# Kernel optimization log

Hardware: AMD Instinct MI355X
Metric: run time of the kernel (lower is better)

## Reference

```python
import jax, jax.numpy as jnp
import numpy as np

N = 1000000
E = 16000000


def gcn_conv(x, W, b, src, dst, dinv_sqrt):
    # x: [N, Cin]; W: [Cin, Cout]; src/dst: [E'] (self-loops included)
    xw = x @ W                                   # [N, Cout]
    norm = dinv_sqrt[src] * dinv_sqrt[dst]       # [E']
    msg = xw[src] * norm[:, None]                # [E', Cout]
    out = jax.ops.segment_sum(msg, dst, num_segments=x.shape[0])
    return out + b


def setup_inputs() -> dict:
    key = jax.random.key(0)
    ks = jax.random.split(key, 8)
    x = jax.random.normal(ks[0], (N, 1), dtype=jnp.float32)
    edge_index = jax.random.randint(ks[1], (2, E), 0, N, dtype=jnp.int64)
    W1 = jax.random.normal(ks[2], (1, 3), dtype=jnp.float32)
    b1 = jax.random.normal(ks[3], (3,), dtype=jnp.float32) * 0.1
    W2 = jax.random.normal(ks[4], (3, 3), dtype=jnp.float32) * 0.5
    b2 = jax.random.normal(ks[5], (3,), dtype=jnp.float32) * 0.1
    W3 = jax.random.normal(ks[6], (3, 3), dtype=jnp.float32) * 0.5
    b3 = jax.random.normal(ks[7], (3,), dtype=jnp.float32) * 0.1
    return {"x": x, "edge_index": edge_index, "W1": W1, "b1": b1,
            "W2": W2, "b2": b2, "W3": W3, "b3": b3}


def reference(x, edge_index, W1, b1, W2, b2, W3, b3):
    n = x.shape[0]
    # add self-loops (PyG GCNConv default)
    loop = jnp.arange(n, dtype=edge_index.dtype)
    src = jnp.concatenate([edge_index[0], loop])
    dst = jnp.concatenate([edge_index[1], loop])
    # symmetric normalization: deg over targets of A + I
    deg = jax.ops.segment_sum(jnp.ones_like(dst, dtype=x.dtype), dst, num_segments=n)
    dinv_sqrt = jnp.where(deg > 0, jax.lax.rsqrt(deg), 0.0)
    h = jax.nn.relu(gcn_conv(x, W1, b1, src, dst, dinv_sqrt))
    h = jax.nn.relu(gcn_conv(h, W2, b2, src, dst, dinv_sqrt))
    h = jax.nn.relu(gcn_conv(h, W3, b3, src, dst, dinv_sqrt))
    return h
```

## Files before the change

### kernel.cpp

```cpp
#include <hip/hip_runtime.h>

#define THREADS 256
#define TILE 8192
#define TPB_S 512
#define EPT 16
#define BUCKET_BITS 10
#define BUCKET_SIZE 1024
#define NT_MAX 2048
#define STAGE_CAP 17152

__device__ __forceinline__ long long llmin(long long a, long long b) { return a < b ? a : b; }


__global__ void detect_i64_kernel(const int* __restrict__ e, int* __restrict__ flag) {
    if (blockIdx.x == 0 && threadIdx.x == 0) {
        bool all_odd_zero = true, any_even = false;
#pragma unroll
        for (int k = 0; k < 16; ++k) {
            if (e[2 * k + 1] != 0) all_odd_zero = false;
            if (e[2 * k] != 0) any_even = true;
        }
        *flag = (all_odd_zero && any_even) ? 1 : 0;
    }
}


__global__ __launch_bounds__(TPB_S) void binsort_kernel(
        const int* __restrict__ e, long long E, const int* __restrict__ flag,
        int nbuck, int* __restrict__ packed, int* __restrict__ ofs) {
    __shared__ int hist[1024];
    __shared__ int sarr[TPB_S];
    __shared__ int srec[TILE];
    const int tid = threadIdx.x;
    hist[tid] = 0;
    hist[tid + TPB_S] = 0;
    __syncthreads();

    const bool i64 = (*flag != 0);
    const long long beg = (long long)blockIdx.x * TILE;
    const int tile_len = (int)llmin((long long)TILE, E - beg);

    int rec[EPT];
    int bkt[EPT];
#pragma unroll
    for (int k = 0; k < EPT; ++k) {
        int j = tid + k * TPB_S;
        bkt[k] = -1;
        if (j < tile_len) {
            long long idx = beg + j;
            int s, d;
            if (i64) { s = ((const int2*)e)[idx].x; d = ((const int2*)e)[E + idx].x; }
            else     { s = e[idx];                  d = e[E + idx]; }
            bkt[k] = d >> BUCKET_BITS;
            rec[k] = ((d & (BUCKET_SIZE - 1)) << 20) | s;
            atomicAdd(&hist[bkt[k]], 1);
        }
    }
    __syncthreads();

    int v0 = hist[2 * tid], v1 = hist[2 * tid + 1];
    sarr[tid] = v0 + v1;
    __syncthreads();
    for (int off = 1; off < TPB_S; off <<= 1) {
        int t = (tid >= off) ? sarr[tid - off] : 0;
        __syncthreads();
        sarr[tid] += t;
        __syncthreads();
    }
    int excl = (tid == 0) ? 0 : sarr[tid - 1];
    hist[2 * tid] = excl;
    hist[2 * tid + 1] = excl + v0;
    __syncthreads();

    int* orow = ofs + (size_t)blockIdx.x * nbuck;
    if (tid < nbuck) orow[tid] = hist[tid];
    if (tid + TPB_S < nbuck) orow[tid + TPB_S] = hist[tid + TPB_S];
    __syncthreads();

#pragma unroll
    for (int k = 0; k < EPT; ++k) {
        if (bkt[k] >= 0) {
            int pos = atomicAdd(&hist[bkt[k]], 1);
            srec[pos] = rec[k];
        }
    }
    __syncthreads();

    int* prow = packed + (size_t)blockIdx.x * TILE;
    for (int j = tid; j < tile_len; j += TPB_S) prow[j] = srec[j];
}

#define TRT 32
__global__ void transpose_kernel(const int* __restrict__ in, int rows, int cols,
                                 int* __restrict__ outT) {
    __shared__ int tb[TRT][TRT + 1];
    int c0 = blockIdx.x * TRT, r0 = blockIdx.y * TRT;
    int lx = threadIdx.x, ly = threadIdx.y;
    for (int dy = ly; dy < TRT; dy += 8) {
        int r = r0 + dy, c = c0 + lx;
        if (r < rows && c < cols) tb[dy][lx] = in[(size_t)r * cols + c];
    }
    __syncthreads();
    for (int dy = ly; dy < TRT; dy += 8) {
        int r = c0 + dy, c = r0 + lx;
        if (r < cols && c < rows) outT[(size_t)r * rows + c] = tb[lx][dy];
    }
}


__global__ __launch_bounds__(THREADS) void bcnt_kernel(
        const int* __restrict__ ofsT, long long E, int ntiles, int nbuck,
        int* __restrict__ bcnt) {
    __shared__ int sh[THREADS];
    const int b = blockIdx.x, tid = threadIdx.x;
    const int* row0 = ofsT + (size_t)b * ntiles;
    const int* row1 = row0 + ntiles;
    const bool last_b = (b == nbuck - 1);
    int s = 0;
    for (int t = tid; t < ntiles; t += THREADS) {
        int o = row0[t];
        int tl = (t == ntiles - 1) ? (int)(E - (long long)t * TILE) : TILE;
        int o2 = last_b ? tl : row1[t];
        s += o2 - o;
    }
    sh[tid] = s;
    __syncthreads();
    for (int off = THREADS >> 1; off > 0; off >>= 1) {
        if (tid < off) sh[tid] += sh[tid + off];
        __syncthreads();
    }
    if (tid == 0) bcnt[b] = sh[0];
}

__global__ __launch_bounds__(1024) void bscan_kernel(
        const int* __restrict__ bcnt, int nbuck, int* __restrict__ bs) {
    __shared__ int sh[1024];
    int tid = threadIdx.x;
    int v = (tid < nbuck) ? bcnt[tid] : 0;
    sh[tid] = v;
    __syncthreads();
    for (int off = 1; off < 1024; off <<= 1) {
        int t = (tid >= off) ? sh[tid - off] : 0;
        __syncthreads();
        sh[tid] += t;
        __syncthreads();
    }
    if (tid < nbuck) bs[tid] = sh[tid] - v;
    if (tid == nbuck - 1) bs[nbuck] = sh[tid];
}


__global__ __launch_bounds__(TPB_S) void merge_kernel(
        const int* __restrict__ ofsT, const int* __restrict__ packed,
        const int* __restrict__ bs, long long E, int ntiles, int nbuck,
        int* __restrict__ merged) {
    __shared__ int lofs[NT_MAX];
    __shared__ int tsum[TPB_S];
    __shared__ int stage[STAGE_CAP];
    const int tid = threadIdx.x, b = blockIdx.x;
    const int* row0 = ofsT + (size_t)b * ntiles;
    const int* row1 = row0 + ntiles;
    const bool last_b = (b == nbuck - 1);
    const int per = (ntiles + TPB_S - 1) / TPB_S;
    const int t0 = tid * per;

    int s = 0;
    for (int k = 0; k < per; ++k) {
        int t = t0 + k;
        if (t < ntiles) {
            int o = row0[t];
            int tl = (t == ntiles - 1) ? (int)(E - (long long)t * TILE) : TILE;
            int o2 = last_b ? tl : row1[t];
            lofs[t] = s;
            s += o2 - o;
        }
    }
    tsum[tid] = s;
    __syncthreads();
    for (int off = 1; off < TPB_S; off <<= 1) {
        int t = (tid >= off) ? tsum[tid - off] : 0;
        __syncthreads();
        tsum[tid] += t;
        __syncthreads();
    }
    const int excl = tsum[tid] - s;
    const int total = tsum[TPB_S - 1];
    for (int k = 0; k < per; ++k) {
        int t = t0 + k;
        if (t < ntiles) lofs[t] += excl;
    }
    __syncthreads();

    const int bsb = bs[b];
    for (int k = 0; k < per; ++k) {
        int t = t0 + k;
        if (t >= ntiles) break;
        int o = row0[t];
        int tl = (t == ntiles - 1) ? (int)(E - (long long)t * TILE) : TILE;
        int o2 = last_b ? tl : row1[t];
        const int* pr = packed + (size_t)t * TILE;
        int q = lofs[t];
        int j = o;
        for (; j + 4 <= o2; j += 4, q += 4) {
            int a0 = pr[j], a1 = pr[j + 1], a2 = pr[j + 2], a3 = pr[j + 3];
            if (q + 3 < STAGE_CAP) {
                stage[q] = a0; stage[q + 1] = a1; stage[q + 2] = a2; stage[q + 3] = a3;
            } else {
                if (q < STAGE_CAP) stage[q] = a0; else merged[bsb + q] = a0;
                if (q + 1 < STAGE_CAP) stage[q + 1] = a1; else merged[bsb + q + 1] = a1;
                if (q + 2 < STAGE_CAP) stage[q + 2] = a2; else merged[bsb + q + 2] = a2;
                merged[bsb + q + 3] = a3;
            }
        }
        for (; j < o2; ++j, ++q) {
            int a0 = pr[j];
            if (q < STAGE_CAP) stage[q] = a0; else merged[bsb + q] = a0;
        }
    }
    __syncthreads();

    const int wlen = total < STAGE_CAP ? total : STAGE_CAP;
    for (int j = tid; j < wlen; j += TPB_S) merged[bsb + j] = stage[j];
}


__global__ void deg_init_kernel(const int* __restrict__ bs, const int* __restrict__ packed,
                                const float* __restrict__ x,
                                float* __restrict__ dinv, float* __restrict__ p, int N) {
    __shared__ int cnt[BUCKET_SIZE];
    for (int k = threadIdx.x; k < BUCKET_SIZE; k += blockDim.x) cnt[k] = 0;
    __syncthreads();
    int beg = bs[blockIdx.x], end = bs[blockIdx.x + 1];
    int stride = blockDim.x;
    int k = beg + threadIdx.x;
    for (; k + 3 * stride < end; k += 4 * stride) {
        unsigned r0 = packed[k], r1 = packed[k + stride];
        unsigned r2 = packed[k + 2 * stride], r3 = packed[k + 3 * stride];
        atomicAdd(&cnt[r0 >> 20], 1);
        atomicAdd(&cnt[r1 >> 20], 1);
        atomicAdd(&cnt[r2 >> 20], 1);
        atomicAdd(&cnt[r3 >> 20], 1);
    }
    for (; k < end; k += stride) atomicAdd(&cnt[((unsigned)packed[k]) >> 20], 1);
    __syncthreads();
    int base = blockIdx.x << BUCKET_BITS;
    for (int j = threadIdx.x; j < BUCKET_SIZE; j += blockDim.x) {
        int i = base + j;
        if (i < N) {
            float di = rsqrtf((float)cnt[j] + 1.0f);
            dinv[i] = di;
            p[i] = x[i] * di;
        }
    }
}

__global__ void layer1_bucket_kernel(const int* __restrict__ bs, const int* __restrict__ packed,
                                     const float* __restrict__ p, const float* __restrict__ dinv,
                                     const float* __restrict__ W1, const float* __restrict__ b1,
                                     const float* __restrict__ W2,
                                     float4* __restrict__ y2, int N) {
    __shared__ float acc[BUCKET_SIZE];
    for (int k = threadIdx.x; k < BUCKET_SIZE; k += blockDim.x) acc[k] = 0.0f;
    __syncthreads();
    int beg = bs[blockIdx.x], end = bs[blockIdx.x + 1];
    int stride = blockDim.x;
    int k = beg + threadIdx.x;
    for (; k + 3 * stride < end; k += 4 * stride) {
        unsigned r0 = packed[k], r1 = packed[k + stride];
        unsigned r2 = packed[k + 2 * stride], r3 = packed[k + 3 * stride];
        float v0 = p[r0 & 0xFFFFFu], v1 = p[r1 & 0xFFFFFu];
        float v2 = p[r2 & 0xFFFFFu], v3 = p[r3 & 0xFFFFFu];
        atomicAdd(&acc[r0 >> 20], v0);
        atomicAdd(&acc[r1 >> 20], v1);
        atomicAdd(&acc[r2 >> 20], v2);
        atomicAdd(&acc[r3 >> 20], v3);
    }
    for (; k < end; k += stride) {
        unsigned rec = (unsigned)packed[k];
        atomicAdd(&acc[rec >> 20], p[rec & 0xFFFFFu]);
    }
    __syncthreads();
    int base = blockIdx.x << BUCKET_BITS;
    for (int j = threadIdx.x; j < BUCKET_SIZE; j += blockDim.x) {
        int i = base + j;
        if (i >= N) continue;
        float di = dinv[i];
        float t = di * (acc[j] + p[i]);
        float h0 = fmaxf(t * W1[0] + b1[0], 0.0f);
        float h1 = fmaxf(t * W1[1] + b1[1], 0.0f);
        float h2 = fmaxf(t * W1[2] + b1[2], 0.0f);
        float4 o;
        o.x = di * (h0 * W2[0] + h1 * W2[3] + h2 * W2[6]);
        o.y = di * (h0 * W2[1] + h1 * W2[4] + h2 * W2[7]);
        o.z = di * (h0 * W2[2] + h1 * W2[5] + h2 * W2[8]);
        o.w = 0.0f;
        y2[i] = o;
    }
}

__global__ void layer_mid_bucket_kernel(const int* __restrict__ bs, const int* __restrict__ packed,
                                        const float4* __restrict__ y, const float* __restrict__ dinv,
                                        const float* __restrict__ b, const float* __restrict__ Wn,
                                        float4* __restrict__ ynext, int N) {
    __shared__ float acc[BUCKET_SIZE * 3];
    for (int k = threadIdx.x; k < BUCKET_SIZE * 3; k += blockDim.x) acc[k] = 0.0f;
    __syncthreads();
    int beg = bs[blockIdx.x], end = bs[blockIdx.x + 1];
    int stride = blockDim.x;
    int k = beg + threadIdx.x;
    for (; k + 3 * stride < end; k += 4 * stride) {
        unsigned r0 = packed[k], r1 = packed[k + stride];
        unsigned r2 = packed[k + 2 * stride], r3 = packed[k + 3 * stride];
        float4 v0 = y[r0 & 0xFFFFFu], v1 = y[r1 & 0xFFFFFu];
        float4 v2 = y[r2 & 0xFFFFFu], v3 = y[r3 & 0xFFFFFu];
        int d0 = (r0 >> 20) * 3, d1 = (r1 >> 20) * 3, d2 = (r2 >> 20) * 3, d3 = (r3 >> 20) * 3;
        atomicAdd(&acc[d0 + 0], v0.x); atomicAdd(&acc[d0 + 1], v0.y); atomicAdd(&acc[d0 + 2], v0.z);
        atomicAdd(&acc[d1 + 0], v1.x); atomicAdd(&acc[d1 + 1], v1.y); atomicAdd(&acc[d1 + 2], v1.z);
        atomicAdd(&acc[d2 + 0], v2.x); atomicAdd(&acc[d2 + 1], v2.y); atomicAdd(&acc[d2 + 2], v2.z);
        atomicAdd(&acc[d3 + 0], v3.x); atomicAdd(&acc[d3 + 1], v3.y); atomicAdd(&acc[d3 + 2], v3.z);
    }
    for (; k < end; k += stride) {
        unsigned rec = (unsigned)packed[k];
        float4 v = y[rec & 0xFFFFFu];
        int dl = (rec >> 20) * 3;
        atomicAdd(&acc[dl + 0], v.x);
        atomicAdd(&acc[dl + 1], v.y);
        atomicAdd(&acc[dl + 2], v.z);
    }
    __syncthreads();
    int base = blockIdx.x << BUCKET_BITS;
    for (int j = threadIdx.x; j < BUCKET_SIZE; j += blockDim.x) {
        int i = base + j;
        if (i >= N) continue;
        float di = dinv[i];
        float4 yi = y[i];
        float h0 = fmaxf(di * (acc[j * 3 + 0] + yi.x) + b[0], 0.0f);
        float h1 = fmaxf(di * (acc[j * 3 + 1] + yi.y) + b[1], 0.0f);
        float h2 = fmaxf(di * (acc[j * 3 + 2] + yi.z) + b[2], 0.0f);
        float4 o;
        o.x = di * (h0 * Wn[0] + h1 * Wn[3] + h2 * Wn[6]);
        o.y = di * (h0 * Wn[1] + h1 * Wn[4] + h2 * Wn[7]);
        o.z = di * (h0 * Wn[2] + h1 * Wn[5] + h2 * Wn[8]);
        o.w = 0.0f;
        ynext[i] = o;
    }
}

__global__ void layer_last_bucket_kernel(const int* __restrict__ bs, const int* __restrict__ packed,
                                         const float4* __restrict__ y, const float* __restrict__ dinv,
                                         const float* __restrict__ b,
                                         float* __restrict__ out, int N) {
    __shared__ float acc[BUCKET_SIZE * 3];
    for (int k = threadIdx.x; k < BUCKET_SIZE * 3; k += blockDim.x) acc[k] = 0.0f;
    __syncthreads();
    int beg = bs[blockIdx.x], end = bs[blockIdx.x + 1];
    int stride = blockDim.x;
    int k = beg + threadIdx.x;
    for (; k + 3 * stride < end; k += 4 * stride) {
        unsigned r0 = packed[k], r1 = packed[k + stride];
        unsigned r2 = packed[k + 2 * stride], r3 = packed[k + 3 * stride];
        float4 v0 = y[r0 & 0xFFFFFu], v1 = y[r1 & 0xFFFFFu];
        float4 v2 = y[r2 & 0xFFFFFu], v3 = y[r3 & 0xFFFFFu];
        int d0 = (r0 >> 20) * 3, d1 = (r1 >> 20) * 3, d2 = (r2 >> 20) * 3, d3 = (r3 >> 20) * 3;
        atomicAdd(&acc[d0 + 0], v0.x); atomicAdd(&acc[d0 + 1], v0.y); atomicAdd(&acc[d0 + 2], v0.z);
        atomicAdd(&acc[d1 + 0], v1.x); atomicAdd(&acc[d1 + 1], v1.y); atomicAdd(&acc[d1 + 2], v1.z);
        atomicAdd(&acc[d2 + 0], v2.x); atomicAdd(&acc[d2 + 1], v2.y); atomicAdd(&acc[d2 + 2], v2.z);
        atomicAdd(&acc[d3 + 0], v3.x); atomicAdd(&acc[d3 + 1], v3.y); atomicAdd(&acc[d3 + 2], v3.z);
    }
    for (; k < end; k += stride) {
        unsigned rec = (unsigned)packed[k];
        float4 v = y[rec & 0xFFFFFu];
        int dl = (rec >> 20) * 3;
        atomicAdd(&acc[dl + 0], v.x);
        atomicAdd(&acc[dl + 1], v.y);
        atomicAdd(&acc[dl + 2], v.z);
    }
    __syncthreads();
    int base = blockIdx.x << BUCKET_BITS;
    for (int j = threadIdx.x; j < BUCKET_SIZE; j += blockDim.x) {
        int i = base + j;
        if (i >= N) continue;
        float di = dinv[i];
        float4 yi = y[i];
        out[i * 3 + 0] = fmaxf(di * (acc[j * 3 + 0] + yi.x) + b[0], 0.0f);
        out[i * 3 + 1] = fmaxf(di * (acc[j * 3 + 1] + yi.y) + b[1], 0.0f);
        out[i * 3 + 2] = fmaxf(di * (acc[j * 3 + 2] + yi.z) + b[2], 0.0f);
    }
}


__global__ void deg_kernel(const int* __restrict__ e, long long E,
                           const int* __restrict__ flag, float* __restrict__ deg) {
    const bool i64 = (*flag != 0);
    long long i = (long long)blockIdx.x * blockDim.x + threadIdx.x;
    const long long stride = (long long)gridDim.x * blockDim.x;
    for (; i < E; i += stride) {
        long long t = i64 ? (long long)e[2 * E + 2 * i] : (long long)e[E + i];
        atomicAdd(deg + t, 1.0f);
    }
}

__global__ void node_init_kernel(const float* __restrict__ x, const float* __restrict__ W1,
                                 float* __restrict__ deg_dinv, float* __restrict__ A, int N) {
    int i = blockIdx.x * blockDim.x + threadIdx.x;
    if (i >= N) return;
    float di = rsqrtf(deg_dinv[i] + 1.0f);
    deg_dinv[i] = di;
    float v = x[i] * di;
    A[i * 3 + 0] = v * W1[0];
    A[i * 3 + 1] = v * W1[1];
    A[i * 3 + 2] = v * W1[2];
}

__global__ void scatter_kernel(const int* __restrict__ e, long long E,
                               const int* __restrict__ flag,
                               const float* __restrict__ y, float* __restrict__ acc) {
    const bool i64 = (*flag != 0);
    long long i = (long long)blockIdx.x * blockDim.x + threadIdx.x;
    const long long stride = (long long)gridDim.x * blockDim.x;
    for (; i < E; i += stride) {
        int s, t;
        if (i64) { s = e[2 * i]; t = e[2 * E + 2 * i]; }
        else     { s = e[i];     t = e[E + i]; }
        atomicAdd(acc + (long long)t * 3 + 0, y[(long long)s * 3 + 0]);
        atomicAdd(acc + (long long)t * 3 + 1, y[(long long)s * 3 + 1]);
        atomicAdd(acc + (long long)t * 3 + 2, y[(long long)s * 3 + 2]);
    }
}

__global__ void finalize_mid_kernel(const float* __restrict__ dinv, const float* __restrict__ y,
                                    float* __restrict__ acc, const float* __restrict__ b,
                                    const float* __restrict__ Wn, int N) {
    int i = blockIdx.x * blockDim.x + threadIdx.x;
    if (i >= N) return;
    float di = dinv[i];
    float h0 = fmaxf(di * (acc[i * 3 + 0] + y[i * 3 + 0]) + b[0], 0.0f);
    float h1 = fmaxf(di * (acc[i * 3 + 1] + y[i * 3 + 1]) + b[1], 0.0f);
    float h2 = fmaxf(di * (acc[i * 3 + 2] + y[i * 3 + 2]) + b[2], 0.0f);
    float z0 = di * (h0 * Wn[0] + h1 * Wn[3] + h2 * Wn[6]);
    float z1 = di * (h0 * Wn[1] + h1 * Wn[4] + h2 * Wn[7]);
    float z2 = di * (h0 * Wn[2] + h1 * Wn[5] + h2 * Wn[8]);
    acc[i * 3 + 0] = z0;
    acc[i * 3 + 1] = z1;
    acc[i * 3 + 2] = z2;
}

__global__ void finalize_last_kernel(const float* __restrict__ dinv, const float* __restrict__ y,
                                     const float* __restrict__ acc, const float* __restrict__ b,
                                     float* __restrict__ out, int N) {
    int i = blockIdx.x * blockDim.x + threadIdx.x;
    if (i >= N) return;
    float di = dinv[i];
    out[i * 3 + 0] = fmaxf(di * (acc[i * 3 + 0] + y[i * 3 + 0]) + b[0], 0.0f);
    out[i * 3 + 1] = fmaxf(di * (acc[i * 3 + 1] + y[i * 3 + 1]) + b[1], 0.0f);
    out[i * 3 + 2] = fmaxf(di * (acc[i * 3 + 2] + y[i * 3 + 2]) + b[2], 0.0f);
}


extern "C" void kernel_launch(void* const* d_in, const int* in_sizes, int n_in,
                              void* d_out, int out_size, void* d_ws, size_t ws_size,
                              hipStream_t stream) {
    const float* x  = (const float*)d_in[0];
    const int*   ei = (const int*)d_in[1];
    const float* W1 = (const float*)d_in[2];
    const float* b1 = (const float*)d_in[3];
    const float* W2 = (const float*)d_in[4];
    const float* b2 = (const float*)d_in[5];
    const float* W3 = (const float*)d_in[6];
    const float* b3 = (const float*)d_in[7];
    float* out = (float*)d_out;

    const long long N = in_sizes[0];
    const long long E = (long long)in_sizes[1] / 2;

    const int nbuck  = (int)((N + BUCKET_SIZE - 1) >> BUCKET_BITS);
    const int ntiles = (int)((E + TILE - 1) / TILE);

    char* w = (char*)d_ws;
    size_t off = 0;
    auto alloc = [&](size_t bytes) -> char* {
        char* pp = w + off;
        off = (off + bytes + 255) & ~(size_t)255;
        return pp;
    };

    int*    flag   = (int*)alloc(4);
    int*    ofs    = (int*)alloc((size_t)ntiles * nbuck * 4);
    int*    ofsT   = (int*)alloc((size_t)nbuck * ntiles * 4);
    int*    bcnt   = (int*)alloc((size_t)nbuck * 4);
    int*    bs     = (int*)alloc(((size_t)nbuck + 1) * 4);
    int*    packed = (int*)alloc((size_t)ntiles * TILE * 4);
    int*    merged = (int*)alloc((size_t)E * 4);
    float*  dinv   = (float*)alloc((size_t)N * 4);
    float*  p      = (float*)alloc((size_t)N * 4);
    float4* y2     = (float4*)packed;
    float4* y3     = (float4*)((char*)packed + (size_t)N * 16);

    const int nblk = (int)((N + THREADS - 1) / THREADS);

    if (off <= ws_size && N <= (1 << 20) && nbuck <= 1024 && ntiles <= NT_MAX &&
        (size_t)ntiles * TILE * 4 >= (size_t)N * 32) {
        detect_i64_kernel<<<1, 64, 0, stream>>>(ei, flag);
        binsort_kernel<<<ntiles, TPB_S, 0, stream>>>(ei, E, flag, nbuck, packed, ofs);
        dim3 tb(32, 8);
        dim3 tg((nbuck + TRT - 1) / TRT, (ntiles + TRT - 1) / TRT);
        transpose_kernel<<<tg, tb, 0, stream>>>(ofs, ntiles, nbuck, ofsT);
        bcnt_kernel<<<nbuck, THREADS, 0, stream>>>(ofsT, E, ntiles, nbuck, bcnt);
        bscan_kernel<<<1, 1024, 0, stream>>>(bcnt, nbuck, bs);
        merge_kernel<<<nbuck, TPB_S, 0, stream>>>(ofsT, packed, bs, E, ntiles, nbuck, merged);

        deg_init_kernel<<<nbuck, THREADS, 0, stream>>>(bs, merged, x, dinv, p, (int)N);
        layer1_bucket_kernel<<<nbuck, THREADS, 0, stream>>>(bs, merged, p, dinv, W1, b1, W2, y2, (int)N);
        layer_mid_bucket_kernel<<<nbuck, THREADS, 0, stream>>>(bs, merged, y2, dinv, b2, W3, y3, (int)N);
        layer_last_bucket_kernel<<<nbuck, THREADS, 0, stream>>>(bs, merged, y3, dinv, b3, out, (int)N);
    } else {
        int*   fflag = (int*)w;
        float* fdinv = (float*)(w + 256);
        float* A     = fdinv + N;
        size_t need_full = 256 + (size_t)N * 4 + (size_t)N * 12 * 2;
        float* B = (ws_size >= need_full) ? (A + 3 * N) : out;
        const int eblk = 2048;

        detect_i64_kernel<<<1, 64, 0, stream>>>(ei, fflag);
        hipMemsetAsync(fdinv, 0, (size_t)N * 4, stream);
        deg_kernel<<<eblk, THREADS, 0, stream>>>(ei, E, fflag, fdinv);
        node_init_kernel<<<nblk, THREADS, 0, stream>>>(x, W1, fdinv, A, (int)N);

        hipMemsetAsync(B, 0, (size_t)N * 12, stream);
        scatter_kernel<<<eblk, THREADS, 0, stream>>>(ei, E, fflag, A, B);
        finalize_mid_kernel<<<nblk, THREADS, 0, stream>>>(fdinv, A, B, b1, W2, (int)N);

        hipMemsetAsync(A, 0, (size_t)N * 12, stream);
        scatter_kernel<<<eblk, THREADS, 0, stream>>>(ei, E, fflag, B, A);
        finalize_mid_kernel<<<nblk, THREADS, 0, stream>>>(fdinv, B, A, b2, W3, (int)N);

        hipMemsetAsync(B, 0, (size_t)N * 12, stream);
        scatter_kernel<<<eblk, THREADS, 0, stream>>>(ei, E, fflag, A, B);
        finalize_last_kernel<<<nblk, THREADS, 0, stream>>>(fdinv, A, B, b3, out, (int)N);
    }
}
```

Measured before the change: 766.8 us.

## Sub-sort merged edges by source slice in LDS and widen bucket kernel blocks

The merge kernel now counts each staged edge record by a coarse source-node slice (8 slices of 128K nodes) and counting-sorts the staged records into a second LDS buffer before writing them out. Within each destination bucket, the edges are then grouped by source range, so the gathers in the layer kernels touch a narrower region of memory and should cache better. The per-bucket aggregation kernels also launch with 512 threads instead of 256. In exchange, the merge kernel gets extra LDS atomics, a second staging buffer and a smaller staging capacity, and it loses its unrolled copy loop.

```diff
diff --git a/kernel.cpp b/kernel.cpp
--- a/kernel.cpp
+++ b/kernel.cpp
@@ -7,7 +7,9 @@
 #define BUCKET_BITS 10
 #define BUCKET_SIZE 1024
 #define NT_MAX 2048
-#define STAGE_CAP 17152
+#define STAGE_CAP 16512
+#define NSLICE 8
+#define SLICE_SHIFT 17
 
 __device__ __forceinline__ long long llmin(long long a, long long b) { return a < b ? a : b; }
 
@@ -157,12 +159,16 @@
     __shared__ int lofs[NT_MAX];
     __shared__ int tsum[TPB_S];
     __shared__ int stage[STAGE_CAP];
+    __shared__ int stage2[STAGE_CAP];
+    __shared__ int scnt[NSLICE];
+    __shared__ int scur[NSLICE];
     const int tid = threadIdx.x, b = blockIdx.x;
     const int* row0 = ofsT + (size_t)b * ntiles;
     const int* row1 = row0 + ntiles;
     const bool last_b = (b == nbuck - 1);
     const int per = (ntiles + TPB_S - 1) / TPB_S;
     const int t0 = tid * per;
+    if (tid < NSLICE) scnt[tid] = 0;
 
     int s = 0;
     for (int k = 0; k < per; ++k) {
@@ -192,6 +198,10 @@
     __syncthreads();
 
     const int bsb = bs[b];
+    int myslc[NSLICE];
+#pragma unroll
+    for (int i = 0; i < NSLICE; ++i) myslc[i] = 0;
+
     for (int k = 0; k < per; ++k) {
         int t = t0 + k;
         if (t >= ntiles) break;
@@ -200,33 +210,43 @@
         int o2 = last_b ? tl : row1[t];
         const int* pr = packed + (size_t)t * TILE;
         int q = lofs[t];
-        int j = o;
-        for (; j + 4 <= o2; j += 4, q += 4) {
-            int a0 = pr[j], a1 = pr[j + 1], a2 = pr[j + 2], a3 = pr[j + 3];
-            if (q + 3 < STAGE_CAP) {
-                stage[q] = a0; stage[q + 1] = a1; stage[q + 2] = a2; stage[q + 3] = a3;
+        for (int j = o; j < o2; ++j, ++q) {
+            int a0 = pr[j];
+            if (q < STAGE_CAP) {
+                stage[q] = a0;
+                myslc[((unsigned)a0 & 0xFFFFFu) >> SLICE_SHIFT]++;
             } else {
-                if (q < STAGE_CAP) stage[q] = a0; else merged[bsb + q] = a0;
-                if (q + 1 < STAGE_CAP) stage[q + 1] = a1; else merged[bsb + q + 1] = a1;
-                if (q + 2 < STAGE_CAP) stage[q + 2] = a2; else merged[bsb + q + 2] = a2;
-                merged[bsb + q + 3] = a3;
+                merged[bsb + q] = a0;
             }
         }
-        for (; j < o2; ++j, ++q) {
-            int a0 = pr[j];
-            if (q < STAGE_CAP) stage[q] = a0; else merged[bsb + q] = a0;
-        }
+    }
+#pragma unroll
+    for (int i = 0; i < NSLICE; ++i)
+        if (myslc[i]) atomicAdd(&scnt[i], myslc[i]);
+    __syncthreads();
+    if (tid == 0) {
+        int run = 0;
+#pragma unroll
+        for (int i = 0; i < NSLICE; ++i) { scur[i] = run; run += scnt[i]; }
     }
     __syncthreads();
 
     const int wlen = total < STAGE_CAP ? total : STAGE_CAP;
-    for (int j = tid; j < wlen; j += TPB_S) merged[bsb + j] = stage[j];
-}
-
-
-__global__ void deg_init_kernel(const int* __restrict__ bs, const int* __restrict__ packed,
-                                const float* __restrict__ x,
-                                float* __restrict__ dinv, float* __restrict__ p, int N) {
+    for (int j = tid; j < wlen; j += TPB_S) {
+        int rec = stage[j];
+        int sl = ((unsigned)rec & 0xFFFFFu) >> SLICE_SHIFT;
+        int pos = atomicAdd(&scur[sl], 1);
+        stage2[pos] = rec;
+    }
+    __syncthreads();
+    for (int j = tid; j < wlen; j += TPB_S) merged[bsb + j] = stage2[j];
+}
+
+
+__global__ __launch_bounds__(TPB_S) void deg_init_kernel(
+        const int* __restrict__ bs, const int* __restrict__ packed,
+        const float* __restrict__ x,
+        float* __restrict__ dinv, float* __restrict__ p, int N) {
     __shared__ int cnt[BUCKET_SIZE];
     for (int k = threadIdx.x; k < BUCKET_SIZE; k += blockDim.x) cnt[k] = 0;
     __syncthreads();
@@ -254,11 +274,12 @@
     }
 }
 
-__global__ void layer1_bucket_kernel(const int* __restrict__ bs, const int* __restrict__ packed,
-                                     const float* __restrict__ p, const float* __restrict__ dinv,
-                                     const float* __restrict__ W1, const float* __restrict__ b1,
-                                     const float* __restrict__ W2,
-                                     float4* __restrict__ y2, int N) {
+__global__ __launch_bounds__(TPB_S) void layer1_bucket_kernel(
+        const int* __restrict__ bs, const int* __restrict__ packed,
+        const float* __restrict__ p, const float* __restrict__ dinv,
+        const float* __restrict__ W1, const float* __restrict__ b1,
+        const float* __restrict__ W2,
+        float4* __restrict__ y2, int N) {
     __shared__ float acc[BUCKET_SIZE];
     for (int k = threadIdx.x; k < BUCKET_SIZE; k += blockDim.x) acc[k] = 0.0f;
     __syncthreads();
@@ -298,10 +319,11 @@
     }
 }
 
-__global__ void layer_mid_bucket_kernel(const int* __restrict__ bs, const int* __restrict__ packed,
-                                        const float4* __restrict__ y, const float* __restrict__ dinv,
-                                        const float* __restrict__ b, const float* __restrict__ Wn,
-                                        float4* __restrict__ ynext, int N) {
+__global__ __launch_bounds__(TPB_S) void layer_mid_bucket_kernel(
+        const int* __restrict__ bs, const int* __restrict__ packed,
+        const float4* __restrict__ y, const float* __restrict__ dinv,
+        const float* __restrict__ b, const float* __restrict__ Wn,
+        float4* __restrict__ ynext, int N) {
     __shared__ float acc[BUCKET_SIZE * 3];
     for (int k = threadIdx.x; k < BUCKET_SIZE * 3; k += blockDim.x) acc[k] = 0.0f;
     __syncthreads();
@@ -346,10 +368,11 @@
     }
 }
 
-__global__ void layer_last_bucket_kernel(const int* __restrict__ bs, const int* __restrict__ packed,
-                                         const float4* __restrict__ y, const float* __restrict__ dinv,
-                                         const float* __restrict__ b,
-                                         float* __restrict__ out, int N) {
+__global__ __launch_bounds__(TPB_S) void layer_last_bucket_kernel(
+        const int* __restrict__ bs, const int* __restrict__ packed,
+        const float4* __restrict__ y, const float* __restrict__ dinv,
+        const float* __restrict__ b,
+        float* __restrict__ out, int N) {
     __shared__ float acc[BUCKET_SIZE * 3];
     for (int k = threadIdx.x; k < BUCKET_SIZE * 3; k += blockDim.x) acc[k] = 0.0f;
     __syncthreads();
@@ -509,10 +532,10 @@
         bscan_kernel<<<1, 1024, 0, stream>>>(bcnt, nbuck, bs);
         merge_kernel<<<nbuck, TPB_S, 0, stream>>>(ofsT, packed, bs, E, ntiles, nbuck, merged);
 
-        deg_init_kernel<<<nbuck, THREADS, 0, stream>>>(bs, merged, x, dinv, p, (int)N);
-        layer1_bucket_kernel<<<nbuck, THREADS, 0, stream>>>(bs, merged, p, dinv, W1, b1, W2, y2, (int)N);
-        layer_mid_bucket_kernel<<<nbuck, THREADS, 0, stream>>>(bs, merged, y2, dinv, b2, W3, y3, (int)N);
-        layer_last_bucket_kernel<<<nbuck, THREADS, 0, stream>>>(bs, merged, y3, dinv, b3, out, (int)N);
+        deg_init_kernel<<<nbuck, TPB_S, 0, stream>>>(bs, merged, x, dinv, p, (int)N);
+        layer1_bucket_kernel<<<nbuck, TPB_S, 0, stream>>>(bs, merged, p, dinv, W1, b1, W2, y2, (int)N);
+        layer_mid_bucket_kernel<<<nbuck, TPB_S, 0, stream>>>(bs, merged, y2, dinv, b2, W3, y3, (int)N);
+        layer_last_bucket_kernel<<<nbuck, TPB_S, 0, stream>>>(bs, merged, y3, dinv, b3, out, (int)N);
     } else {
         int*   fflag = (int*)w;
         float* fdinv = (float*)(w + 256);
```

Measured after the change: 904.9 us. 18.0% more time.
